# Optimization experiments

Hardware: AMD Instinct MI355X
Metric: run time of the kernel (lower is better)

The kernel has to match this reference:

```python
import jax, jax.numpy as jnp
import numpy as np

IN_DIM = 512
RATIO = 8
QK_DIM = IN_DIM // RATIO  # 64
B, C, H, W = 8, IN_DIM, 64, 64


def setup_inputs() -> dict:
    key = jax.random.key(0)
    ks = jax.random.split(key, 9)
    x = jax.random.normal(ks[0], (B, C, H, W), dtype=jnp.float32)
    y = jax.random.normal(ks[1], (B, C, H, W), dtype=jnp.float32)
    z = jax.random.normal(ks[2], (B, C, H, W), dtype=jnp.float32)
    # 1x1 conv weights, xavier_normal with gain=0.02: std = gain*sqrt(2/(fan_in+fan_out))
    def xavier(k, out_c, in_c, gain=0.02):
        std = gain * np.sqrt(2.0 / (in_c + out_c))
        return jax.random.normal(k, (out_c, in_c), dtype=jnp.float32) * std
    Wq = xavier(ks[3], QK_DIM, C)
    Wk = xavier(ks[4], QK_DIM, C)
    Wv = xavier(ks[5], C, C)
    bq = jnp.zeros((QK_DIM,), dtype=jnp.float32)
    bk = jnp.zeros((QK_DIM,), dtype=jnp.float32)
    bv = jnp.zeros((C,), dtype=jnp.float32)
    gamma = jnp.zeros((1,), dtype=jnp.float32)
    return {"x": x, "y": y, "z": z, "Wq": Wq, "bq": bq, "Wk": Wk,
            "bk": bk, "Wv": Wv, "bv": bv, "gamma": gamma}


def reference(x, y, z, Wq, bq, Wk, bk, Wv, bv, gamma):
    b, c, h, w = x.shape
    n = h * w
    # 1x1 convs == per-pixel linear projections
    q = (jnp.einsum('oc,bchw->bohw', Wq, x) + bq[None, :, None, None]).reshape(b, -1, n)  # [B, d, N]
    k = (jnp.einsum('oc,bchw->bohw', Wk, y) + bk[None, :, None, None]).reshape(b, -1, n)  # [B, d, N]
    v = (jnp.einsum('oc,bchw->bohw', Wv, z) + bv[None, :, None, None]).reshape(b, -1, n)  # [B, C, N]
    # energy[b, i, j] = <q[:, i], k[:, j]>, no scaling (matches original)
    energy = jnp.einsum('bdn,bdm->bnm', q, k)      # [B, N, N]
    attention = jax.nn.softmax(energy, axis=-1)     # softmax over keys
    # out = value @ attention^T : out[:, c, i] = sum_j v[:, c, j] * attention[:, i, j]
    out = jnp.einsum('bcj,bij->bci', v, attention)  # [B, C, N]
    out = out.reshape(b, c, h, w)
    out = gamma[0] * out + x
    return out
```

## Files before the change

### kernel.cpp

```cpp
#include <hip/hip_runtime.h>
#include <hip/hip_bf16.h>
#include <hip/hip_fp8.h>
#include <stdint.h>

#define B_   8
#define C_   512
#define NPIX 4096
#define VLDB 4160

typedef __attribute__((ext_vector_type(8))) short bf16x8;
typedef __attribute__((ext_vector_type(4))) float f32x4;

__device__ __forceinline__ uint16_t f2bf(float f) {
    union { float f; uint32_t u; } v; v.f = f;
    uint32_t u = v.u;
    return (uint16_t)((u + 0x7FFFu + ((u >> 16) & 1u)) >> 16);
}

__device__ __forceinline__ uint32_t pk2(float a, float b) {
    union { __hip_bfloat162 h; uint32_t u; } c;
    c.h = __float22bfloat162_rn(make_float2(a, b));
    return c.u;
}

__device__ __forceinline__ float fexp2(float x) {
#if __has_builtin(__builtin_amdgcn_exp2f)
    return __builtin_amdgcn_exp2f(x);
#else
    return exp2f(x);
#endif
}

template<bool HI>
__device__ __forceinline__ uint32_t pk_fp8(float a, float b, uint32_t old) {
#if __has_builtin(__builtin_amdgcn_cvt_pk_fp8_f32)
    return __builtin_amdgcn_cvt_pk_fp8_f32(a, b, old, HI);
#else
    union { __hip_fp8_storage_t s[4]; uint32_t u; } r; r.u = old;
    r.s[HI * 2 + 0] = __hip_cvt_float_to_fp8(a, __HIP_SATFINITE, __HIP_E4M3);
    r.s[HI * 2 + 1] = __hip_cvt_float_to_fp8(b, __HIP_SATFINITE, __HIP_E4M3);
    return r.u;
#endif
}
__device__ __forceinline__ uint8_t f2fp8(float a) {
#if __has_builtin(__builtin_amdgcn_cvt_pk_fp8_f32)
    uint32_t u = __builtin_amdgcn_cvt_pk_fp8_f32(a, 0.f, 0u, false);
    return (uint8_t)(u & 0xFF);
#else
    return __hip_cvt_float_to_fp8(a, __HIP_SATFINITE, __HIP_E4M3);
#endif
}

__device__ __forceinline__ int perm64(int d) {
    return ((d >> 3) & 3) * 16 + ((d >> 5) << 3) + (d & 7);
}

__global__ __launch_bounds__(256, 4) void convw_kernel(
    const float* __restrict__ W, uint16_t* __restrict__ Wb)
{
    int i = (blockIdx.x * 256 + threadIdx.x) * 8;
    float4 a = *(const float4*)&W[i];
    float4 b = *(const float4*)&W[i + 4];
    union { bf16x8 v; uint32_t u[4]; } r;
    r.u[0] = pk2(a.x, a.y); r.u[1] = pk2(a.z, a.w);
    r.u[2] = pk2(b.x, b.y); r.u[3] = pk2(b.z, b.w);
    *(bf16x8*)&Wb[i] = r.v;
}

__global__ __launch_bounds__(256, 2) void proj_kernel(
    const float* __restrict__ X, const float* __restrict__ W,
    const float* __restrict__ bias, uint16_t* __restrict__ out,
    float scale)
{
    __shared__ char xt[64 * 128];
    const int b  = blockIdx.z;
    const int n0 = blockIdx.x * 64;
    const int t = threadIdx.x, w = t >> 6, l = t & 63;
    const int l15 = l & 15, lg = l >> 4;
    const float* Xb = X + (size_t)b * C_ * NPIX + n0;

    f32x4 acc[4] = {};

    for (int cc = 0; cc < C_; cc += 64) {
        __syncthreads();
        #pragma unroll
        for (int i = 0; i < 16; i += 2) {
            int c = w * 16 + i;
            float f0 = Xb[(size_t)(cc + c) * NPIX + l];
            float f1 = Xb[(size_t)(cc + c + 1) * NPIX + l];
            uint32_t pair = pk2(f0, f1);
            int byte = (l * 128 + c * 2) ^ ((l & 7) << 4);
            *(uint32_t*)(xt + byte) = pair;
        }
        __syncthreads();
        #pragma unroll
        for (int kk = 0; kk < 2; kk++) {
            int o  = w * 16 + l15;
            int cb = cc + kk * 32 + lg * 8;
            float4 wa = *(const float4*)&W[(size_t)o * C_ + cb];
            float4 wb = *(const float4*)&W[(size_t)o * C_ + cb + 4];
            union { bf16x8 v; uint32_t u[4]; } afu;
            afu.u[0] = pk2(wa.x, wa.y); afu.u[1] = pk2(wa.z, wa.w);
            afu.u[2] = pk2(wb.x, wb.y); afu.u[3] = pk2(wb.z, wb.w);
            #pragma unroll
            for (int jt = 0; jt < 4; jt++) {
                int n = jt * 16 + l15;
                int byte = (n * 128 + (kk * 32 + lg * 8) * 2) ^ ((n & 7) << 4);
                bf16x8 bfr = *(bf16x8*)(xt + byte);
                acc[jt] = __builtin_amdgcn_mfma_f32_16x16x32_bf16(afu.v, bfr, acc[jt], 0, 0, 0);
            }
        }
    }
    int og = w * 16 + lg * 4;
    #pragma unroll
    for (int jt = 0; jt < 4; jt++) {
        int n = n0 + jt * 16 + l15;
        #pragma unroll
        for (int r = 0; r < 4; r++) {
            float v = (acc[jt][r] + bias[og + r]) * scale;
            out[((size_t)b * NPIX + n) * 64 + og + r] = f2bf(v);
        }
    }
}

__global__ __launch_bounds__(256, 1) void projv_kernel(
    const float* __restrict__ X, const uint16_t* __restrict__ Wb,
    const float* __restrict__ bias, uint8_t* __restrict__ outp)
{
    __shared__ char xt[2][64 * 1024];
    const int b  = blockIdx.z;
    const int ng = blockIdx.x;
    const int t = threadIdx.x, w = t >> 6, l = t & 63;
    const int l15 = l & 15, lg = l >> 4;

    #pragma unroll
    for (int nt = 0; nt < 2; nt++) {
        const float* Xb = X + (size_t)b * C_ * NPIX + (ng * 2 + nt) * 64;
        for (int cc = 0; cc < C_; cc += 64) {
            #pragma unroll
            for (int i = 0; i < 16; i += 2) {
                int c = cc + w * 16 + i;
                float f0 = Xb[(size_t)c * NPIX + l];
                float f1 = Xb[(size_t)(c + 1) * NPIX + l];
                uint32_t pair = pk2(f0, f1);
                int byte = (l * 1024 + c * 2) ^ ((l & 7) << 4);
                *(uint32_t*)(xt[nt] + byte) = pair;
            }
        }
    }
    __syncthreads();

    #pragma unroll 1
    for (int o0 = 0; o0 < C_; o0 += 64) {
        f32x4 acc[2][4] = {};
        #pragma unroll 1
        for (int cc = 0; cc < C_; cc += 64) {
            #pragma unroll
            for (int kk = 0; kk < 2; kk++) {
                int o  = o0 + w * 16 + l15;
                int cb = cc + kk * 32 + lg * 8;
                bf16x8 af = *(const bf16x8*)&Wb[(size_t)o * C_ + cb];
                #pragma unroll
                for (int nt = 0; nt < 2; nt++)
                    #pragma unroll
                    for (int jt = 0; jt < 4; jt++) {
                        int n = jt * 16 + l15;
                        int byte = (n * 1024 + cb * 2) ^ ((n & 7) << 4);
                        bf16x8 bfr = *(bf16x8*)(xt[nt] + byte);
                        acc[nt][jt] = __builtin_amdgcn_mfma_f32_16x16x32_bf16(af, bfr, acc[nt][jt], 0, 0, 0);
                    }
            }
        }
        int og = o0 + w * 16 + lg * 4;
        #pragma unroll
        for (int nt = 0; nt < 2; nt++) {
            int n0 = (ng * 2 + nt) * 64;
            #pragma unroll
            for (int jt = 0; jt < 4; jt++) {
                int j6 = jt * 16 + l15;
                int pos = perm64(j6);
                #pragma unroll
                for (int r = 0; r < 4; r++) {
                    float v = (acc[nt][jt][r] + bias[og + r]) * 64.0f;
                    outp[((size_t)b * C_ + og + r) * (size_t)VLDB + (size_t)(n0 >> 6) * 64 + pos] = f2fp8(v);
                }
            }
        }
    }
}

__global__ __launch_bounds__(512, 1) void attn_kernel(
    const uint16_t* __restrict__ qT, const uint16_t* __restrict__ kT,
    const uint8_t* __restrict__ vB, const float* __restrict__ X,
    const float* __restrict__ gamma_p, float* __restrict__ out)
{
    __shared__ char  Pl[3][64 * 128];
    __shared__ float lsum[64][9];

    const int id = blockIdx.x;
    const int b  = id & 7;
    const int qt = id >> 3;
    const int i0 = qt * 64;

    const int t = threadIdx.x, w = t >> 6, l = t & 63;
    const int l15 = l & 15, lg = l >> 4;
    const int c0 = w * 64;

    auto barrier_lds = [&]() {
        asm volatile("s_waitcnt lgkmcnt(0)" ::: "memory");
        __builtin_amdgcn_s_barrier();
    };

    bf16x8 q8[4][2];
    #pragma unroll
    for (int it = 0; it < 4; it++)
        #pragma unroll
        for (int kk = 0; kk < 2; kk++)
            q8[it][kk] = *(const bf16x8*)&qT[((size_t)b * NPIX + i0 + it*16 + l15) * 64 + kk*32 + lg*8];

    f32x4 oacc[4][4] = {};
    float l_part[4] = {0.f, 0.f, 0.f, 0.f};

    const uint16_t* kTb = kT + (size_t)b * NPIX * 64;
    const uint8_t*  vBb = vB + ((size_t)b * C_ + c0) * (size_t)VLDB + lg * 16;
    const uint16_t* kROW = kTb + (size_t)(w * 16 + l15) * 64 + lg * 8;

    int vrowB[4];
    #pragma unroll
    for (int ct = 0; ct < 4; ct++) vrowB[ct] = (ct * 16 + l15) * VLDB;

    bf16x8 k8[2];
    ulong2 vreg[8];
    f32x4 s[4];

    auto loadK = [&](int step) {
        const uint16_t* p = kROW + (size_t)step * (128 * 64);
        k8[0] = *(const bf16x8*)p;
        k8[1] = *(const bf16x8*)(p + 32);
    };
    auto loadV = [&](int step) {
        const uint8_t* p = vBb + (size_t)step * 128;
        #pragma unroll
        for (int jh = 0; jh < 2; jh++)
            #pragma unroll
            for (int ct = 0; ct < 4; ct++)
                vreg[jh*4+ct] = *(const ulong2*)(p + vrowB[ct] + jh * 64);
    };
    auto QK = [&]() {
        #pragma unroll
        for (int it = 0; it < 4; it++) s[it] = f32x4{0.f, 0.f, 0.f, 0.f};
        __builtin_amdgcn_s_setprio(1);
        #pragma unroll
        for (int kk = 0; kk < 2; kk++)
            #pragma unroll
            for (int it = 0; it < 4; it++)
                s[it] = __builtin_amdgcn_mfma_f32_16x16x32_bf16(k8[kk], q8[it][kk], s[it], 0, 0, 0);
        __builtin_amdgcn_s_setprio(0);
    };
    auto PcomputeWrite = [&](char* Pn) {
        #pragma unroll
        for (int it = 0; it < 4; it++) {
            float e0 = fexp2(fminf(s[it][0], 60.f));
            float e1 = fexp2(fminf(s[it][1], 60.f));
            float e2 = fexp2(fminf(s[it][2], 60.f));
            float e3 = fexp2(fminf(s[it][3], 60.f));
            l_part[it] += (e0 + e1) + (e2 + e3);
            uint32_t p4 = pk_fp8<false>(e0, e1, 0u);
            p4 = pk_fp8<true>(e2, e3, p4);
            int i = it * 16 + l15;
            int byte = (i * 128 + w * 16 + lg * 4) ^ ((i & 15) << 3);
            *(uint32_t*)(Pn + byte) = p4;
        }
    };
    auto PV = [&](const char* P) {
        __builtin_amdgcn_s_setprio(1);
        #pragma unroll
        for (int jh = 0; jh < 2; jh++)
            #pragma unroll
            for (int kk = 0; kk < 2; kk++) {
                long pb[4];
                #pragma unroll
                for (int it = 0; it < 4; it++) {
                    int i = it * 16 + l15;
                    int byte = (i * 128 + jh * 64 + kk * 32 + lg * 8) ^ ((i & 15) << 3);
                    pb[it] = *(const long*)(P + byte);
                }
                #pragma unroll
                for (int ct = 0; ct < 4; ct++) {
                    long v8 = (long)(kk ? vreg[jh*4+ct].y : vreg[jh*4+ct].x);
                    #pragma unroll
                    for (int it = 0; it < 4; it++)
                        oacc[ct][it] = __builtin_amdgcn_mfma_f32_16x16x32_fp8_fp8(v8, pb[it], oacc[ct][it], 0, 0, 0);
                }
            }
        __builtin_amdgcn_s_setprio(0);
    };

    loadK(0);
    loadV(0);
    QK();
    loadK(1);
    PcomputeWrite(Pl[0]);
    QK();
    loadK(2);
    PcomputeWrite(Pl[1]);

    char* Pprev = Pl[0];
    char* Pcur  = Pl[1];
    char* Pnext = Pl[2];

    #pragma unroll 1
    for (int jt_ = 1; jt_ < 32; ++jt_) {
        barrier_lds();
        PV(Pprev);
        loadV(jt_);
        if (jt_ < 31) {
            QK();
            if (jt_ < 30) loadK(jt_ + 2);
            PcomputeWrite(Pnext);
        }
        char* tmp = Pprev; Pprev = Pcur; Pcur = Pnext; Pnext = tmp;
    }
    barrier_lds();
    PV(Pprev);

    #pragma unroll
    for (int it = 0; it < 4; it++) {
        float v = l_part[it];
        v += __shfl_xor(v, 16);
        v += __shfl_xor(v, 32);
        if (lg == 0) lsum[it * 16 + l15][w] = v;
    }
    __syncthreads();

    float gamma = gamma_p[0];
    float rl[4];
    #pragma unroll
    for (int it = 0; it < 4; it++) {
        int i = it * 16 + l15;
        float lt = ((lsum[i][0] + lsum[i][1]) + (lsum[i][2] + lsum[i][3]))
                 + ((lsum[i][4] + lsum[i][5]) + (lsum[i][6] + lsum[i][7]));
        rl[it] = 1.0f / (64.0f * lt);
    }
    #pragma unroll
    for (int ct = 0; ct < 4; ct++)
        #pragma unroll
        for (int r = 0; r < 4; r++) {
            int c = c0 + ct * 16 + lg * 4 + r;
            #pragma unroll
            for (int it = 0; it < 4; it++) {
                int n = i0 + it * 16 + l15;
                size_t idx = ((size_t)b * C_ + c) * NPIX + n;
                out[idx] = gamma * (oacc[ct][it][r] * rl[it]) + X[idx];
            }
        }
}

extern "C" void kernel_launch(void* const* d_in, const int* in_sizes, int n_in,
                              void* d_out, int out_size, void* d_ws, size_t ws_size,
                              hipStream_t stream) {
    const float* x     = (const float*)d_in[0];
    const float* y     = (const float*)d_in[1];
    const float* z     = (const float*)d_in[2];
    const float* Wq    = (const float*)d_in[3];
    const float* bq    = (const float*)d_in[4];
    const float* Wk    = (const float*)d_in[5];
    const float* bk    = (const float*)d_in[6];
    const float* Wv    = (const float*)d_in[7];
    const float* bv    = (const float*)d_in[8];
    const float* gamma = (const float*)d_in[9];
    float* out = (float*)d_out;

    uint16_t* qT  = (uint16_t*)d_ws;
    uint16_t* kT  = qT + (size_t)B_ * NPIX * 64;
    uint8_t*  vb  = (uint8_t*)(kT + (size_t)B_ * NPIX * 64);
    uint16_t* Wvb = (uint16_t*)(vb + (size_t)B_ * C_ * VLDB);

    convw_kernel<<<dim3(128), dim3(256), 0, stream>>>(Wv, Wvb);
    proj_kernel <<<dim3(64, 1, 8), dim3(256), 0, stream>>>(x, Wq, bq, qT, 1.4426950408889634f);
    proj_kernel <<<dim3(64, 1, 8), dim3(256), 0, stream>>>(y, Wk, bk, kT, 1.0f);
    projv_kernel<<<dim3(32, 1, 8), dim3(256), 0, stream>>>(z, Wvb, bv, vb);
    attn_kernel <<<dim3(512), dim3(512), 0, stream>>>(qT, kT, vb, x, gamma, out);
}
```

Before: 257.6 us.

## Fuse Q, K and V projections into one kernel sharing LDS staging

Replaces the three projection launches (two Q/K kernels and a V kernel) with a single kernel that stages x, y, then z into the same 64 KB LDS tile and computes Q, K and V for a 64-pixel block in sequence. V projection now uses 64-pixel blocks (512 blocks) instead of 128-pixel blocks (256 blocks), which improves occupancy but halves reuse of each loaded Wv fragment. The goal is to cut launch overhead and run Q/K work at the same parallelism as V. In exchange, each block serializes three phases with full-tile staging, and the Q/K phases now pay for 64 KB of LDS per block.

```diff
diff --git a/kernel.cpp b/kernel.cpp
--- a/kernel.cpp
+++ b/kernel.cpp
@@ -67,75 +67,23 @@
     *(bf16x8*)&Wb[i] = r.v;
 }
 
-__global__ __launch_bounds__(256, 2) void proj_kernel(
-    const float* __restrict__ X, const float* __restrict__ W,
-    const float* __restrict__ bias, uint16_t* __restrict__ out,
-    float scale)
+__global__ __launch_bounds__(256, 2) void proj_all_kernel(
+    const float* __restrict__ x, const float* __restrict__ y,
+    const float* __restrict__ z,
+    const float* __restrict__ Wq, const float* __restrict__ bq,
+    const float* __restrict__ Wk, const float* __restrict__ bk,
+    const uint16_t* __restrict__ Wvb, const float* __restrict__ bv,
+    uint16_t* __restrict__ qT, uint16_t* __restrict__ kT,
+    uint8_t* __restrict__ vb)
 {
-    __shared__ char xt[64 * 128];
-    const int b  = blockIdx.z;
+    __shared__ char xt[64 * 1024];
+    const int b  = blockIdx.y;
     const int n0 = blockIdx.x * 64;
     const int t = threadIdx.x, w = t >> 6, l = t & 63;
     const int l15 = l & 15, lg = l >> 4;
-    const float* Xb = X + (size_t)b * C_ * NPIX + n0;
-
-    f32x4 acc[4] = {};
-
-    for (int cc = 0; cc < C_; cc += 64) {
-        __syncthreads();
-        #pragma unroll
-        for (int i = 0; i < 16; i += 2) {
-            int c = w * 16 + i;
-            float f0 = Xb[(size_t)(cc + c) * NPIX + l];
-            float f1 = Xb[(size_t)(cc + c + 1) * NPIX + l];
-            uint32_t pair = pk2(f0, f1);
-            int byte = (l * 128 + c * 2) ^ ((l & 7) << 4);
-            *(uint32_t*)(xt + byte) = pair;
-        }
-        __syncthreads();
-        #pragma unroll
-        for (int kk = 0; kk < 2; kk++) {
-            int o  = w * 16 + l15;
-            int cb = cc + kk * 32 + lg * 8;
-            float4 wa = *(const float4*)&W[(size_t)o * C_ + cb];
-            float4 wb = *(const float4*)&W[(size_t)o * C_ + cb + 4];
-            union { bf16x8 v; uint32_t u[4]; } afu;
-            afu.u[0] = pk2(wa.x, wa.y); afu.u[1] = pk2(wa.z, wa.w);
-            afu.u[2] = pk2(wb.x, wb.y); afu.u[3] = pk2(wb.z, wb.w);
-            #pragma unroll
-            for (int jt = 0; jt < 4; jt++) {
-                int n = jt * 16 + l15;
-                int byte = (n * 128 + (kk * 32 + lg * 8) * 2) ^ ((n & 7) << 4);
-                bf16x8 bfr = *(bf16x8*)(xt + byte);
-                acc[jt] = __builtin_amdgcn_mfma_f32_16x16x32_bf16(afu.v, bfr, acc[jt], 0, 0, 0);
-            }
-        }
-    }
-    int og = w * 16 + lg * 4;
-    #pragma unroll
-    for (int jt = 0; jt < 4; jt++) {
-        int n = n0 + jt * 16 + l15;
-        #pragma unroll
-        for (int r = 0; r < 4; r++) {
-            float v = (acc[jt][r] + bias[og + r]) * scale;
-            out[((size_t)b * NPIX + n) * 64 + og + r] = f2bf(v);
-        }
-    }
-}
-
-__global__ __launch_bounds__(256, 1) void projv_kernel(
-    const float* __restrict__ X, const uint16_t* __restrict__ Wb,
-    const float* __restrict__ bias, uint8_t* __restrict__ outp)
-{
-    __shared__ char xt[2][64 * 1024];
-    const int b  = blockIdx.z;
-    const int ng = blockIdx.x;
-    const int t = threadIdx.x, w = t >> 6, l = t & 63;
-    const int l15 = l & 15, lg = l >> 4;
-
-    #pragma unroll
-    for (int nt = 0; nt < 2; nt++) {
-        const float* Xb = X + (size_t)b * C_ * NPIX + (ng * 2 + nt) * 64;
+
+    auto stage = [&](const float* X) {
+        const float* Xb = X + (size_t)b * C_ * NPIX + n0;
         for (int cc = 0; cc < C_; cc += 64) {
             #pragma unroll
             for (int i = 0; i < 16; i += 2) {
@@ -144,46 +92,84 @@
                 float f1 = Xb[(size_t)(c + 1) * NPIX + l];
                 uint32_t pair = pk2(f0, f1);
                 int byte = (l * 1024 + c * 2) ^ ((l & 7) << 4);
-                *(uint32_t*)(xt[nt] + byte) = pair;
-            }
-        }
-    }
-    __syncthreads();
-
+                *(uint32_t*)(xt + byte) = pair;
+            }
+        }
+    };
+
+    auto qkphase = [&](const float* W, const float* bias, float scale,
+                       uint16_t* out) {
+        f32x4 acc[4] = {};
+        #pragma unroll 1
+        for (int cc = 0; cc < C_; cc += 64) {
+            #pragma unroll
+            for (int kk = 0; kk < 2; kk++) {
+                int o  = w * 16 + l15;
+                int cb = cc + kk * 32 + lg * 8;
+                float4 wa = *(const float4*)&W[(size_t)o * C_ + cb];
+                float4 wb = *(const float4*)&W[(size_t)o * C_ + cb + 4];
+                union { bf16x8 v; uint32_t u[4]; } afu;
+                afu.u[0] = pk2(wa.x, wa.y); afu.u[1] = pk2(wa.z, wa.w);
+                afu.u[2] = pk2(wb.x, wb.y); afu.u[3] = pk2(wb.z, wb.w);
+                #pragma unroll
+                for (int jt = 0; jt < 4; jt++) {
+                    int n = jt * 16 + l15;
+                    int byte = (n * 1024 + cb * 2) ^ ((n & 7) << 4);
+                    bf16x8 bfr = *(bf16x8*)(xt + byte);
+                    acc[jt] = __builtin_amdgcn_mfma_f32_16x16x32_bf16(afu.v, bfr, acc[jt], 0, 0, 0);
+                }
+            }
+        }
+        int og = w * 16 + lg * 4;
+        #pragma unroll
+        for (int jt = 0; jt < 4; jt++) {
+            int n = n0 + jt * 16 + l15;
+            #pragma unroll
+            for (int r = 0; r < 4; r++) {
+                float v = (acc[jt][r] + bias[og + r]) * scale;
+                out[((size_t)b * NPIX + n) * 64 + og + r] = f2bf(v);
+            }
+        }
+    };
+
+    stage(x);
+    __syncthreads();
+    qkphase(Wq, bq, 1.4426950408889634f, qT);
+    __syncthreads();
+    stage(y);
+    __syncthreads();
+    qkphase(Wk, bk, 1.0f, kT);
+    __syncthreads();
+    stage(z);
+    __syncthreads();
     #pragma unroll 1
     for (int o0 = 0; o0 < C_; o0 += 64) {
-        f32x4 acc[2][4] = {};
+        f32x4 acc[4] = {};
         #pragma unroll 1
         for (int cc = 0; cc < C_; cc += 64) {
             #pragma unroll
             for (int kk = 0; kk < 2; kk++) {
                 int o  = o0 + w * 16 + l15;
                 int cb = cc + kk * 32 + lg * 8;
-                bf16x8 af = *(const bf16x8*)&Wb[(size_t)o * C_ + cb];
+                bf16x8 af = *(const bf16x8*)&Wvb[(size_t)o * C_ + cb];
                 #pragma unroll
-                for (int nt = 0; nt < 2; nt++)
-                    #pragma unroll
-                    for (int jt = 0; jt < 4; jt++) {
-                        int n = jt * 16 + l15;
-                        int byte = (n * 1024 + cb * 2) ^ ((n & 7) << 4);
-                        bf16x8 bfr = *(bf16x8*)(xt[nt] + byte);
-                        acc[nt][jt] = __builtin_amdgcn_mfma_f32_16x16x32_bf16(af, bfr, acc[nt][jt], 0, 0, 0);
-                    }
+                for (int jt = 0; jt < 4; jt++) {
+                    int n = jt * 16 + l15;
+                    int byte = (n * 1024 + cb * 2) ^ ((n & 7) << 4);
+                    bf16x8 bfr = *(bf16x8*)(xt + byte);
+                    acc[jt] = __builtin_amdgcn_mfma_f32_16x16x32_bf16(af, bfr, acc[jt], 0, 0, 0);
+                }
             }
         }
         int og = o0 + w * 16 + lg * 4;
         #pragma unroll
-        for (int nt = 0; nt < 2; nt++) {
-            int n0 = (ng * 2 + nt) * 64;
-            #pragma unroll
-            for (int jt = 0; jt < 4; jt++) {
-                int j6 = jt * 16 + l15;
-                int pos = perm64(j6);
-                #pragma unroll
-                for (int r = 0; r < 4; r++) {
-                    float v = (acc[nt][jt][r] + bias[og + r]) * 64.0f;
-                    outp[((size_t)b * C_ + og + r) * (size_t)VLDB + (size_t)(n0 >> 6) * 64 + pos] = f2fp8(v);
-                }
+        for (int jt = 0; jt < 4; jt++) {
+            int j6 = jt * 16 + l15;
+            int pos = perm64(j6);
+            #pragma unroll
+            for (int r = 0; r < 4; r++) {
+                float v = (acc[jt][r] + bv[og + r]) * 64.0f;
+                vb[((size_t)b * C_ + og + r) * (size_t)VLDB + (size_t)(n0 >> 6) * 64 + pos] = f2fp8(v);
             }
         }
     }
@@ -377,8 +363,7 @@
     uint16_t* Wvb = (uint16_t*)(vb + (size_t)B_ * C_ * VLDB);
 
     convw_kernel<<<dim3(128), dim3(256), 0, stream>>>(Wv, Wvb);
-    proj_kernel <<<dim3(64, 1, 8), dim3(256), 0, stream>>>(x, Wq, bq, qT, 1.4426950408889634f);
-    proj_kernel <<<dim3(64, 1, 8), dim3(256), 0, stream>>>(y, Wk, bk, kT, 1.0f);
-    projv_kernel<<<dim3(32, 1, 8), dim3(256), 0, stream>>>(z, Wvb, bv, vb);
-    attn_kernel <<<dim3(512), dim3(512), 0, stream>>>(qT, kT, vb, x, gamma, out);
-}
+    proj_all_kernel<<<dim3(64, 8), dim3(256), 0, stream>>>(
+        x, y, z, Wq, bq, Wk, bk, Wvb, bv, qT, kT, vb);
+    attn_kernel<<<dim3(512), dim3(512), 0, stream>>>(qT, kT, vb, x, gamma, out);
+}
```

Result: faster. 245.6 us (-4.7%).
